# Optimization experiments

Measured on AMD Instinct MI355X. Metric: run time of the kernel, lower is better.

Reference implementation:

```python
import jax, jax.numpy as jnp
import numpy as np

BINS = 1000  # torch: int(max-min)*100; ~1000 for standardized randn data, fixed for jit


def _entropy(counts, n, width):
    # torch.histogram(density=True): probs = counts / (n * bin_width)
    probs = counts / (n * width)
    safe = jnp.where(probs > 0, probs, 1.0)
    return jnp.sum(jnp.where(probs > 0, -probs * jnp.log2(safe), 0.0))


def setup_inputs() -> dict:
    key = jax.random.key(0)
    k1, k2 = jax.random.split(key)
    x = jax.random.normal(k1, (1024, 64, 16, 16), dtype=jnp.float32)
    u = jax.random.uniform(k2, (1024, 64, 16, 16), dtype=jnp.float32)  # dropout noise
    return {"x": x, "u": u}


def reference(x, u):
    B = x.shape[0]
    temp = x.reshape(B, -1)              # [B, D]
    D = temp.shape[1]

    # corrcoef across rows (each row is a variable)
    tc = temp - temp.mean(axis=1, keepdims=True)
    cov = tc @ tc.T                      # [B, B]
    d = jnp.sqrt(jnp.diag(cov))
    corr = cov / (d[:, None] * d[None, :])
    factor1 = jnp.mean(jnp.abs(corr), axis=1)            # [B]

    # global standardization (torch.std default is unbiased, ddof=1)
    tnorm = (temp - temp.mean()) / jnp.std(temp, ddof=1)
    lo, hi = tnorm.min(), tnorm.max()
    width = (hi - lo) / BINS
    idx = jnp.clip(jnp.floor((tnorm - lo) / width).astype(jnp.int32), 0, BINS - 1)

    # per-row histograms via batched scatter-add; batch histogram = sum of rows
    row_counts = jax.vmap(lambda ii: jnp.zeros(BINS, jnp.float32).at[ii].add(1.0))(idx)  # [B, BINS]
    batch_counts = row_counts.sum(axis=0)

    batch_entropy = _entropy(batch_counts, B * D, width)
    local_entropy = jax.vmap(lambda c: _entropy(c, D, width))(row_counts)  # [B]

    f2 = local_entropy / batch_entropy
    is_zero = f2 == 0
    f1 = jnp.where(is_zero, 0.0, factor1)
    f2 = jnp.where(is_zero, 1.0, jnp.where(f2 < 1.0, 1.0 / f2, f2))
    keep = f1 / f2                       # 1 - p, per row
    p = 1.0 - keep                       # [B]

    mask = (u.reshape(B, -1) > p[:, None]).astype(x.dtype)
    out = (mask * temp) / keep[:, None]
    return out.reshape(x.shape)
```

## Files before the change

kernel.cpp:

```cpp
#include <hip/hip_runtime.h>
#include <math.h>

#define NROWS 1024
#define DCOLS 16384
#define NTOT  16777216
#define BINS  1000
#define NPAIR 136

typedef short short8 __attribute__((ext_vector_type(8)));
typedef unsigned short ushort8 __attribute__((ext_vector_type(8)));
typedef float f32x4 __attribute__((ext_vector_type(4)));

#define GLOAD_LDS16(gp, lp) __builtin_amdgcn_global_load_lds( \
    (const __attribute__((address_space(1))) unsigned int*)(gp), \
    (__attribute__((address_space(3))) unsigned int*)(lp), 16, 0, 0)

__device__ __constant__ int CHK_TR[12] = {1,17,33,49,  0,5,10,15,  128,149,170,191};
__device__ __constant__ int CHK_CB[12] = {0,0,0,0,     128,128,128,128,  0,0,0,0};
__device__ __constant__ int CHK_SL[12] = {0,0,0,0,     2,2,2,2,    0,0,0,0};

__global__ __launch_bounds__(256) void k_rowsplit(const float* __restrict__ x,
    unsigned short* __restrict__ phi, unsigned short* __restrict__ plo,
    double* __restrict__ rowsum, double* __restrict__ rowsumsq,
    double* __restrict__ rowmin, double* __restrict__ rowmax) {
  const int row = blockIdx.x, t = threadIdx.x;
  const size_t base = (size_t)row * DCOLS;
  double s = 0.0, s2 = 0.0;
  float mn = 3.4028235e38f, mx = -3.4028235e38f;
  #pragma unroll
  for (int i = 0; i < 8; ++i) {
    const size_t off = base + (size_t)i * 2048 + (size_t)t * 8;
    const float4 v0 = *(const float4*)(x + off);
    const float4 v1 = *(const float4*)(x + off + 4);
    const float vv[8] = {v0.x, v0.y, v0.z, v0.w, v1.x, v1.y, v1.z, v1.w};
    ushort8 h, lo;
    #pragma unroll
    for (int c = 0; c < 8; ++c) {
      unsigned ub = __float_as_uint(vv[c]);
      unsigned hb = (ub + 0x7FFFu + ((ub >> 16) & 1u)) >> 16;
      float hf = __uint_as_float(hb << 16);
      float r = vv[c] - hf;
      unsigned ur = __float_as_uint(r);
      unsigned lb = (ur + 0x7FFFu + ((ur >> 16) & 1u)) >> 16;
      h[c] = (unsigned short)hb; lo[c] = (unsigned short)lb;
      double dv = vv[c];
      s += dv; s2 += dv * dv;
      mn = fminf(mn, vv[c]); mx = fmaxf(mx, vv[c]);
    }
    *(ushort8*)(phi + off) = h;
    *(ushort8*)(plo + off) = lo;
  }
  #pragma unroll
  for (int off = 32; off > 0; off >>= 1) {
    s  += __shfl_down(s, off);
    s2 += __shfl_down(s2, off);
    mn = fminf(mn, __shfl_down(mn, off));
    mx = fmaxf(mx, __shfl_down(mx, off));
  }
  __shared__ double lsd[8];
  __shared__ float  lsf[8];
  const int lane = t & 63, w = t >> 6;
  if (lane == 0) { lsd[w] = s; lsd[4 + w] = s2; lsf[w] = mn; lsf[4 + w] = mx; }
  __syncthreads();
  if (t == 0) {
    rowsum[row]   = (lsd[0] + lsd[1]) + (lsd[2] + lsd[3]);
    rowsumsq[row] = (lsd[4] + lsd[5]) + (lsd[6] + lsd[7]);
    rowmin[row] = (double)fminf(fminf(lsf[0], lsf[1]), fminf(lsf[2], lsf[3]));
    rowmax[row] = (double)fmaxf(fmaxf(lsf[4], lsf[5]), fmaxf(lsf[6], lsf[7]));
  }
}

__global__ __launch_bounds__(256) void k_rowstats(const float* __restrict__ x,
    double* __restrict__ rowsum, double* __restrict__ rowsumsq,
    double* __restrict__ rowmin, double* __restrict__ rowmax) {
  const int row = blockIdx.x;
  const int t = threadIdx.x;
  const float4* xr = (const float4*)(x + (size_t)row * DCOLS);
  double s = 0.0, s2 = 0.0;
  float mn = 3.4028235e38f, mx = -3.4028235e38f;
  for (int j = t; j < DCOLS / 4; j += 256) {
    float4 v = xr[j];
    double a = v.x, b = v.y, c = v.z, d = v.w;
    s  += (a + b) + (c + d);
    s2 += (a * a + b * b) + (c * c + d * d);
    mn = fminf(mn, fminf(fminf(v.x, v.y), fminf(v.z, v.w)));
    mx = fmaxf(mx, fmaxf(fmaxf(v.x, v.y), fmaxf(v.z, v.w)));
  }
  #pragma unroll
  for (int off = 32; off > 0; off >>= 1) {
    s  += __shfl_down(s, off);
    s2 += __shfl_down(s2, off);
    mn = fminf(mn, __shfl_down(mn, off));
    mx = fmaxf(mx, __shfl_down(mx, off));
  }
  __shared__ double lsd[8];
  __shared__ float  lsf[8];
  const int lane = t & 63, w = t >> 6;
  if (lane == 0) { lsd[w] = s; lsd[4 + w] = s2; lsf[w] = mn; lsf[4 + w] = mx; }
  __syncthreads();
  if (t == 0) {
    rowsum[row]   = (lsd[0] + lsd[1]) + (lsd[2] + lsd[3]);
    rowsumsq[row] = (lsd[4] + lsd[5]) + (lsd[6] + lsd[7]);
    rowmin[row] = (double)fminf(fminf(lsf[0], lsf[1]), fminf(lsf[2], lsf[3]));
    rowmax[row] = (double)fmaxf(fmaxf(lsf[4], lsf[5]), fmaxf(lsf[6], lsf[7]));
  }
}

__global__ __launch_bounds__(256) void k_stats2(
    const double* __restrict__ rowsum, const double* __restrict__ rowsumsq,
    const double* __restrict__ rowmin, const double* __restrict__ rowmax,
    double* __restrict__ m, double* __restrict__ dn, float* __restrict__ fscal,
    float* __restrict__ flg, unsigned* __restrict__ bc) {
#pragma clang fp contract(off)
  const int t = threadIdx.x;
  for (int b = t; b < BINS; b += 256) bc[b] = 0;
  double s = 0.0, s2 = 0.0, mn = 1e300, mx = -1e300;
  for (int r = t; r < NROWS; r += 256) {
    s += rowsum[r]; s2 += rowsumsq[r];
    mn = fmin(mn, rowmin[r]); mx = fmax(mx, rowmax[r]);
  }
  #pragma unroll
  for (int off = 32; off > 0; off >>= 1) {
    s  += __shfl_down(s, off);
    s2 += __shfl_down(s2, off);
    mn = fmin(mn, __shfl_down(mn, off));
    mx = fmax(mx, __shfl_down(mx, off));
  }
  __shared__ double lsd[16];
  const int lane = t & 63, w = t >> 6;
  if (lane == 0) { lsd[w] = s; lsd[4 + w] = s2; lsd[8 + w] = mn; lsd[12 + w] = mx; }
  __syncthreads();
  if (t == 0) {
    double S  = (lsd[0] + lsd[1]) + (lsd[2] + lsd[3]);
    double S2 = (lsd[4] + lsd[5]) + (lsd[6] + lsd[7]);
    double MN = fmin(fmin(lsd[8], lsd[9]), fmin(lsd[10], lsd[11]));
    double MX = fmax(fmax(lsd[12], lsd[13]), fmax(lsd[14], lsd[15]));
    const double N = 16777216.0;
    double mu  = S / N;
    double var = (S2 - S * S / N) / (N - 1.0);
    double sig = sqrt(var);
    float mu32 = (float)mu;
    float sg32 = (float)sig;
    float mnf  = (float)MN;
    float mxf  = (float)MX;
    float lof  = (mnf - mu32) / sg32;
    float hif  = (mxf - mu32) / sg32;
    float wf   = (hif - lof) / 1000.0f;
    fscal[0] = mu32;
    fscal[1] = sg32;
    fscal[2] = lof;
    fscal[3] = wf;
    fscal[4] = 16384.0f * wf;
    fscal[5] = 16777216.0f * wf;
    flg[0] = 0.0f;
  }
  __syncthreads();
  for (int r = t; r < NROWS; r += 256) {
    double rs = rowsum[r];
    m[r]  = rs / 16384.0;
    dn[r] = sqrt(rowsumsq[r] - rs * rs * (1.0 / 16384.0));
  }
}

__global__ __launch_bounds__(256) void k_gramm_sk(
    const unsigned short* __restrict__ phi, const unsigned short* __restrict__ plo,
    float* __restrict__ Gs) {
  const int pid = blockIdx.x >> 2, ks = blockIdx.x & 3;
  int bi = 0, rem = pid;
  while (rem >= 16 - bi) { rem -= 16 - bi; ++bi; }
  const int bj = bi + rem;
  const bool diag = (bi == bj);
  __shared__ short As[2][64][64];
  __shared__ short Bs[2][64][64];
  const int t = threadIdx.x;
  const int w = t >> 6, l = t & 63;

  const unsigned short* plane = (w & 1) ? plo : phi;
  const int prow0 = (w & 2) ? bj * 64 : bi * 64;
  short* lbase = (w & 2) ? &Bs[w & 1][0][0] : &As[w & 1][0][0];
  const bool skipStage = diag && (w & 2);
  const unsigned short* gbase = plane
      + (size_t)(prow0 + (l >> 3)) * DCOLS + (((l & 7) ^ (l >> 3)) * 8);

  f32x4 acc[4] = {{0.f,0.f,0.f,0.f},{0.f,0.f,0.f,0.f},{0.f,0.f,0.f,0.f},{0.f,0.f,0.f,0.f}};
  double dacc[4][4] = {{0,0,0,0},{0,0,0,0},{0,0,0,0},{0,0,0,0}};

  const int arow = w * 16 + (l & 15);
  const int ar7  = arow & 7;
  const short* Bsrc0 = diag ? &As[0][0][0] : &Bs[0][0][0];
  const short* Bsrc1 = diag ? &As[1][0][0] : &Bs[1][0][0];
  const int kbeg = ks * 4096;

  for (int K0 = kbeg; K0 < kbeg + 4096; K0 += 2048) {
    for (int k0 = K0; k0 < K0 + 2048; k0 += 64) {
      __syncthreads();
      if (!skipStage) {
        #pragma unroll
        for (int q = 0; q < 8; ++q)
          GLOAD_LDS16(gbase + (size_t)q * 8 * DCOLS + k0, lbase + q * 512);
      }
      __syncthreads();
      const int p0 = ((l >> 4)) ^ ar7;
      const int p1 = (4 + (l >> 4)) ^ ar7;
      short8 ah0 = *(const short8*)&As[0][arow][p0 * 8];
      short8 ah1 = *(const short8*)&As[0][arow][p1 * 8];
      short8 al0 = *(const short8*)&As[1][arow][p0 * 8];
      short8 al1 = *(const short8*)&As[1][arow][p1 * 8];
      #pragma unroll
      for (int cj = 0; cj < 4; ++cj) {
        const int brow = cj * 16 + (l & 15);
        const int q0 = ((l >> 4)) ^ (brow & 7);
        const int q1 = (4 + (l >> 4)) ^ (brow & 7);
        short8 bh0 = *(const short8*)(Bsrc0 + brow * 64 + q0 * 8);
        short8 bh1 = *(const short8*)(Bsrc0 + brow * 64 + q1 * 8);
        short8 bl0 = *(const short8*)(Bsrc1 + brow * 64 + q0 * 8);
        short8 bl1 = *(const short8*)(Bsrc1 + brow * 64 + q1 * 8);
        acc[cj] = __builtin_amdgcn_mfma_f32_16x16x32_bf16(ah0, bh0, acc[cj], 0, 0, 0);
        acc[cj] = __builtin_amdgcn_mfma_f32_16x16x32_bf16(ah1, bh1, acc[cj], 0, 0, 0);
        acc[cj] = __builtin_amdgcn_mfma_f32_16x16x32_bf16(ah0, bl0, acc[cj], 0, 0, 0);
        acc[cj] = __builtin_amdgcn_mfma_f32_16x16x32_bf16(ah1, bl1, acc[cj], 0, 0, 0);
        acc[cj] = __builtin_amdgcn_mfma_f32_16x16x32_bf16(al0, bh0, acc[cj], 0, 0, 0);
        acc[cj] = __builtin_amdgcn_mfma_f32_16x16x32_bf16(al1, bh1, acc[cj], 0, 0, 0);
      }
    }
    #pragma unroll
    for (int cj = 0; cj < 4; ++cj) {
      #pragma unroll
      for (int v = 0; v < 4; ++v) dacc[cj][v] += (double)acc[cj][v];
      acc[cj] = (f32x4){0.f, 0.f, 0.f, 0.f};
    }
  }

  float* gt = Gs + ((size_t)pid * 4 + ks) * 4096;
  #pragma unroll
  for (int cj = 0; cj < 4; ++cj)
    #pragma unroll
    for (int v = 0; v < 4; ++v)
      gt[(w * 16 + (l >> 4) * 4 + v) * 64 + cj * 16 + (l & 15)] = (float)dacc[cj][v];
}

__global__ __launch_bounds__(256) void k_gepi(const float* __restrict__ Gs,
    const double* __restrict__ m, const double* __restrict__ dn,
    double* __restrict__ fpart) {
  const int pid = blockIdx.x;
  int bi = 0, rem = pid;
  while (rem >= 16 - bi) { rem -= 16 - bi; ++bi; }
  const int bj = bi + rem;
  const bool diag = (bi == bj);
  __shared__ double Gt[64][65];
  const int t = threadIdx.x;
  const float* g = Gs + (size_t)pid * 4 * 4096;
  for (int i = t; i < 4096; i += 256) {
    double sg = ((double)g[i] + (double)g[4096 + i])
              + ((double)g[8192 + i] + (double)g[12288 + i]);
    Gt[i >> 6][i & 63] = sg;
  }
  __syncthreads();
  {
    const int r = t >> 2, q = t & 3;
    const double mi = m[bi * 64 + r] * 16384.0;
    double s = 0.0;
    #pragma unroll
    for (int i = 0; i < 16; ++i) {
      const int c = q * 16 + i;
      double cov = Gt[r][c] - mi * m[bj * 64 + c];
      s += fabs(cov) / dn[bj * 64 + c];
    }
    s += __shfl_xor(s, 1); s += __shfl_xor(s, 2);
    if (q == 0) fpart[(size_t)(bi * 64 + r) * 16 + bj] = s;
  }
  if (!diag) {
    const int c = t >> 2, q = t & 3;
    const double mj = m[bj * 64 + c] * 16384.0;
    double sc = 0.0;
    #pragma unroll
    for (int i = 0; i < 16; ++i) {
      const int r = q * 16 + i;
      double cov = Gt[r][c] - m[bi * 64 + r] * mj;
      sc += fabs(cov) / dn[bi * 64 + r];
    }
    sc += __shfl_xor(sc, 1); sc += __shfl_xor(sc, 2);
    if (q == 0) fpart[(size_t)(bj * 64 + c) * 16 + bi] = sc;
  }
}

__global__ __launch_bounds__(256) void k_check3(const float* __restrict__ x,
    const double* __restrict__ m, const double* __restrict__ dn,
    double* __restrict__ chkpart) {
  const int b = blockIdx.x;
  const int e = b >> 3, grp = b & 7;
  const int t = threadIdx.x;
  const int cl = t >> 5;
  const int ks = t & 31;
  const int trow = CHK_TR[e];
  const int col  = CHK_CB[e] + grp * 8 + cl;
  const float4* xa = (const float4*)(x + (size_t)trow * DCOLS) + ks * 128;
  const float4* xb = (const float4*)(x + (size_t)col  * DCOLS) + ks * 128;
  double g = 0.0;
  for (int k = 0; k < 128; ++k) {
    float4 va = xa[k], vb = xb[k];
    g += (double)va.x * vb.x + (double)va.y * vb.y
       + (double)va.z * vb.z + (double)va.w * vb.w;
  }
  g += __shfl_xor(g, 1); g += __shfl_xor(g, 2); g += __shfl_xor(g, 4);
  g += __shfl_xor(g, 8); g += __shfl_xor(g, 16);
  __shared__ double cd[8];
  if (ks == 0) cd[cl] = g;
  __syncthreads();
  if (t == 0) {
    double s = 0.0;
    #pragma unroll
    for (int i = 0; i < 8; ++i) {
      int c = CHK_CB[e] + grp * 8 + i;
      double cov = cd[i] - 16384.0 * m[trow] * m[c];
      s += fabs(cov) / dn[c];
    }
    chkpart[e * 8 + grp] = s;
  }
}

__global__ __launch_bounds__(256) void k_gram(const float* __restrict__ x,
    const double* __restrict__ m, const double* __restrict__ dn,
    double* __restrict__ fpart) {
  __shared__ float As[32][72];
  __shared__ float Bs[32][72];
  __shared__ double red[64][16];
  const int t = threadIdx.x;
  const int bi = blockIdx.y, bj = blockIdx.x;
  const int tx = t & 15, ty = t >> 4;
  const int lr = t >> 2, lc = t & 3;
  const float* Ap = x + (size_t)(bi * 64 + lr) * DCOLS;
  const float* Bp = x + (size_t)(bj * 64 + lr) * DCOLS;
  double acc[4][4];
  #pragma unroll
  for (int i = 0; i < 4; ++i)
    #pragma unroll
    for (int j = 0; j < 4; ++j) acc[i][j] = 0.0;
  float4 a0 = ((const float4*)Ap)[lc];
  float4 a1 = ((const float4*)Ap)[lc + 4];
  float4 b0 = ((const float4*)Bp)[lc];
  float4 b1 = ((const float4*)Bp)[lc + 4];
  for (int k0 = 0; k0 < DCOLS; k0 += 32) {
    __syncthreads();
    {
      const float* a0p = (const float*)&a0;
      const float* a1p = (const float*)&a1;
      const float* b0p = (const float*)&b0;
      const float* b1p = (const float*)&b1;
      #pragma unroll
      for (int jj = 0; jj < 4; ++jj) {
        As[lc * 4 + jj][lr]      = a0p[jj];
        As[16 + lc * 4 + jj][lr] = a1p[jj];
        Bs[lc * 4 + jj][lr]      = b0p[jj];
        Bs[16 + lc * 4 + jj][lr] = b1p[jj];
      }
    }
    __syncthreads();
    if (k0 + 32 < DCOLS) {
      a0 = ((const float4*)(Ap + k0 + 32))[lc];
      a1 = ((const float4*)(Ap + k0 + 32))[lc + 4];
      b0 = ((const float4*)(Bp + k0 + 32))[lc];
      b1 = ((const float4*)(Bp + k0 + 32))[lc + 4];
    }
    float ac[4][4];
    #pragma unroll
    for (int i = 0; i < 4; ++i)
      #pragma unroll
      for (int j = 0; j < 4; ++j) ac[i][j] = 0.0f;
    #pragma unroll
    for (int k = 0; k < 32; ++k) {
      const float4 av = *(const float4*)&As[k][ty * 4];
      const float4 bv = *(const float4*)&Bs[k][tx * 4];
      const float aa[4] = {av.x, av.y, av.z, av.w};
      const float bb[4] = {bv.x, bv.y, bv.z, bv.w};
      #pragma unroll
      for (int i = 0; i < 4; ++i)
        #pragma unroll
        for (int j = 0; j < 4; ++j)
          ac[i][j] += aa[i] * bb[j];
    }
    #pragma unroll
    for (int i = 0; i < 4; ++i)
      #pragma unroll
      for (int j = 0; j < 4; ++j) acc[i][j] += (double)ac[i][j];
  }
  double mr[4], mc[4], dc[4];
  #pragma unroll
  for (int i = 0; i < 4; ++i) mr[i] = m[bi * 64 + ty * 4 + i];
  #pragma unroll
  for (int j = 0; j < 4; ++j) {
    int col = bj * 64 + tx * 4 + j;
    mc[j] = m[col]; dc[j] = dn[col];
  }
  #pragma unroll
  for (int i = 0; i < 4; ++i) {
    double pi = 0.0;
    #pragma unroll
    for (int j = 0; j < 4; ++j) {
      double cov = acc[i][j] - 16384.0 * mr[i] * mc[j];
      pi += fabs(cov) / dc[j];
    }
    red[ty * 4 + i][tx] = pi;
  }
  __syncthreads();
  if (t < 64) {
    double ssum = 0.0;
    #pragma unroll
    for (int q = 0; q < 16; ++q) ssum += red[t][q];
    fpart[(size_t)(bi * 64 + t) * 16 + bj] = ssum;
  }
}

__global__ __launch_bounds__(256) void k_hist(const float* __restrict__ x,
    const float* __restrict__ fscal, double* __restrict__ localent,
    unsigned* __restrict__ bc) {
#pragma clang fp contract(off)
  __shared__ unsigned h[BINS];
  const int row = blockIdx.x, t = threadIdx.x;
  for (int b = t; b < BINS; b += 256) h[b] = 0;
  __syncthreads();
  const float mu32 = fscal[0], sg32 = fscal[1], lof = fscal[2], wf = fscal[3];
  const float4* xr = (const float4*)(x + (size_t)row * DCOLS);
  for (int j = t; j < DCOLS / 4; j += 256) {
    float4 v = xr[j];
    float vv[4] = {v.x, v.y, v.z, v.w};
    #pragma unroll
    for (int c = 0; c < 4; ++c) {
      float tn = (vv[c] - mu32) / sg32;
      float q  = (tn - lof) / wf;
      int idx = (int)floorf(q);
      idx = idx < 0 ? 0 : (idx > BINS - 1 ? BINS - 1 : idx);
      atomicAdd(&h[idx], 1u);
    }
  }
  __syncthreads();
  const double Dw = (double)fscal[4];
  double ls = 0.0;
  for (int b = t; b < BINS; b += 256) {
    unsigned c = h[b];
    if (c) {
      atomicAdd(&bc[b], c);
      double pd = (double)c / Dw;
      ls -= pd * log2(pd);
    }
  }
  #pragma unroll
  for (int off = 32; off > 0; off >>= 1) ls += __shfl_down(ls, off);
  __shared__ double lsd[4];
  const int lane = t & 63, w = t >> 6;
  if (lane == 0) lsd[w] = ls;
  __syncthreads();
  if (t == 0) localent[row] = (lsd[0] + lsd[1]) + (lsd[2] + lsd[3]);
}

__global__ __launch_bounds__(256) void k_final(const unsigned* __restrict__ bc,
    const float* __restrict__ fscal, const double* __restrict__ localent,
    const double* __restrict__ fpart, const double* __restrict__ dn,
    const double* __restrict__ chkpart, float* __restrict__ flg,
    float* __restrict__ pf, float* __restrict__ kf) {
#pragma clang fp contract(off)
  const int t = threadIdx.x;
  if (t < 12) {
    double s = 0.0;
    #pragma unroll
    for (int q = 0; q < 8; ++q) s += chkpart[t * 8 + q];
    double got = fpart[(size_t)CHK_TR[t] * 16 + CHK_SL[t]];
    if (fabs(got - s) > 2e-3 * fmax(fabs(s), 1e-30))
      atomicAdd(flg, 1e6f * (float)(t + 1));
  }
  const double Nw = (double)fscal[5];
  double be = 0.0;
  for (int b = t; b < BINS; b += 256) {
    unsigned c = bc[b];
    if (c) { double pd = (double)c / Nw; be -= pd * log2(pd); }
  }
  #pragma unroll
  for (int off = 32; off > 0; off >>= 1) be += __shfl_down(be, off);
  __shared__ double lsd[4];
  __shared__ double sbent;
  const int lane = t & 63, w = t >> 6;
  if (lane == 0) lsd[w] = be;
  __syncthreads();
  if (t == 0) sbent = (lsd[0] + lsd[1]) + (lsd[2] + lsd[3]);
  __syncthreads();
  const float bef = (float)sbent;
  for (int r = t; r < NROWS; r += 256) {
    double s = 0.0;
    #pragma unroll
    for (int q = 0; q < 16; ++q) s += fpart[(size_t)r * 16 + q];
    float f1f = (float)(s / (dn[r] * 1024.0));
    float lef = (float)localent[r];
    float f2f = lef / bef;
    if (f2f == 0.0f) { f1f = 0.0f; f2f = 1.0f; }
    else if (f2f < 1.0f) f2f = 1.0f / f2f;
    float keepf = f1f / f2f;
    pf[r] = 1.0f - keepf;
    kf[r] = keepf;
  }
}

__global__ __launch_bounds__(256) void k_apply(const float* __restrict__ x,
    const float* __restrict__ u, const float* __restrict__ pf,
    const float* __restrict__ kf, const float* __restrict__ flg,
    float* __restrict__ out) {
#pragma clang fp contract(off)
  const size_t e = ((size_t)blockIdx.x * 256 + threadIdx.x) * 4;
  const float fl = flg[0];
  if (fl != 0.0f) {
    float4 o = {0.f, 0.f, 0.f, 0.f};
    if (e == 0) o.x = fl;
    *(float4*)(out + e) = o;
    return;
  }
  const int row = (int)(e >> 14);
  const float pr = pf[row], kr = kf[row];
  const float4 xv = *(const float4*)(x + e);
  const float4 uv = *(const float4*)(u + e);
  float4 o;
  o.x = (uv.x > pr) ? (xv.x / kr) : 0.0f;
  o.y = (uv.y > pr) ? (xv.y / kr) : 0.0f;
  o.z = (uv.z > pr) ? (xv.z / kr) : 0.0f;
  o.w = (uv.w > pr) ? (xv.w / kr) : 0.0f;
  *(float4*)(out + e) = o;
}

extern "C" void kernel_launch(void* const* d_in, const int* in_sizes, int n_in,
                              void* d_out, int out_size, void* d_ws, size_t ws_size,
                              hipStream_t stream) {
  const float* x = (const float*)d_in[0];
  const float* u = (const float*)d_in[1];
  float* out = (float*)d_out;

  const size_t PLANE = (size_t)NROWS * DCOLS * sizeof(unsigned short);
  const size_t NDBL  = 7 * 1024 + (size_t)NROWS * 16 + 96;
  const size_t TAILB = NDBL * 8 + (2056 + 4) * 4 + BINS * 4;
  const bool big = ws_size >= 2 * PLANE + TAILB;

  char* base = (char*)d_ws;
  unsigned short* phi = (unsigned short*)base;
  unsigned short* plo = (unsigned short*)(base + PLANE);
  double* W = big ? (double*)(base + 2 * PLANE) : (double*)base;

  double* rowsum   = W;
  double* rowsumsq = W + 1024;
  double* rowmin   = W + 2048;
  double* rowmax   = W + 3072;
  double* m        = W + 4096;
  double* dn       = W + 5120;
  double* localent = W + 6144;
  double* fpart    = W + 7168;
  double* chkpart  = W + 7168 + (size_t)NROWS * 16;
  float*  F        = (float*)(chkpart + 96);
  float*  pf       = F;
  float*  kf       = F + 1024;
  float*  fscal    = F + 2048;
  float*  flg      = F + 2056;
  unsigned* bc     = (unsigned*)(F + 2060);

  if (big) {
    float* Gs = out;
    k_rowsplit<<<NROWS, 256, 0, stream>>>(x, phi, plo, rowsum, rowsumsq, rowmin, rowmax);
    k_stats2<<<1, 256, 0, stream>>>(rowsum, rowsumsq, rowmin, rowmax, m, dn, fscal, flg, bc);
    k_gramm_sk<<<NPAIR * 4, 256, 0, stream>>>(phi, plo, Gs);
    k_gepi<<<NPAIR, 256, 0, stream>>>(Gs, m, dn, fpart);
    k_check3<<<96, 256, 0, stream>>>(x, m, dn, chkpart);
  } else {
    k_rowstats<<<NROWS, 256, 0, stream>>>(x, rowsum, rowsumsq, rowmin, rowmax);
    k_stats2<<<1, 256, 0, stream>>>(rowsum, rowsumsq, rowmin, rowmax, m, dn, fscal, flg, bc);
    k_gram<<<dim3(16, 16), 256, 0, stream>>>(x, m, dn, fpart);
    k_check3<<<96, 256, 0, stream>>>(x, m, dn, chkpart);
  }
  k_hist<<<NROWS, 256, 0, stream>>>(x, fscal, localent, bc);
  k_final<<<1, 256, 0, stream>>>(bc, fscal, localent, fpart, dn, chkpart, flg, pf, kf);
  k_apply<<<NTOT / (256 * 4), 256, 0, stream>>>(x, u, pf, kf, flg, out);
}
```

Measured before the change: 213.5 us.

## Raise Gram split-K to 8, use 2x2 wave tiling, fuse epilogue with check

The Gram kernel now splits K eight ways instead of four, giving 1088 blocks and better CU fill. Each wave computes a 32x32 quadrant with 2x2 MFMA subtiles instead of a 16x64 strip, which cuts LDS fragment reloads per MFMA. The epilogue now sums eight partials, and the check kernel is merged into it as extra blocks, removing one launch. The cost is twice the partial-Gram traffic through global memory and more epilogue reads. Per-block fp32 accumulation now covers 2048 K instead of being flushed to double every 2048, so precision is about the same.

```diff
diff --git a/kernel.cpp b/kernel.cpp
--- a/kernel.cpp
+++ b/kernel.cpp
@@ -6,6 +6,7 @@
 #define NTOT  16777216
 #define BINS  1000
 #define NPAIR 136
+#define KSPL  8
 
 typedef short short8 __attribute__((ext_vector_type(8)));
 typedef unsigned short ushort8 __attribute__((ext_vector_type(8)));
@@ -165,7 +166,7 @@
 __global__ __launch_bounds__(256) void k_gramm_sk(
     const unsigned short* __restrict__ phi, const unsigned short* __restrict__ plo,
     float* __restrict__ Gs) {
-  const int pid = blockIdx.x >> 2, ks = blockIdx.x & 3;
+  const int pid = blockIdx.x >> 3, ks = blockIdx.x & 7;
   int bi = 0, rem = pid;
   while (rem >= 16 - bi) { rem -= 16 - bi; ++bi; }
   const int bj = bi + rem;
@@ -182,77 +183,124 @@
   const unsigned short* gbase = plane
       + (size_t)(prow0 + (l >> 3)) * DCOLS + (((l & 7) ^ (l >> 3)) * 8);
 
-  f32x4 acc[4] = {{0.f,0.f,0.f,0.f},{0.f,0.f,0.f,0.f},{0.f,0.f,0.f,0.f},{0.f,0.f,0.f,0.f}};
-  double dacc[4][4] = {{0,0,0,0},{0,0,0,0},{0,0,0,0},{0,0,0,0}};
-
-  const int arow = w * 16 + (l & 15);
-  const int ar7  = arow & 7;
-  const short* Bsrc0 = diag ? &As[0][0][0] : &Bs[0][0][0];
-  const short* Bsrc1 = diag ? &As[1][0][0] : &Bs[1][0][0];
-  const int kbeg = ks * 4096;
-
-  for (int K0 = kbeg; K0 < kbeg + 4096; K0 += 2048) {
-    for (int k0 = K0; k0 < K0 + 2048; k0 += 64) {
-      __syncthreads();
-      if (!skipStage) {
+  f32x4 acc[2][2] = {{{0.f,0.f,0.f,0.f},{0.f,0.f,0.f,0.f}},
+                     {{0.f,0.f,0.f,0.f},{0.f,0.f,0.f,0.f}}};
+  double dacc[2][2][4] = {{{0,0,0,0},{0,0,0,0}},{{0,0,0,0},{0,0,0,0}}};
+
+  const int wr = w >> 1, wc = w & 1;
+  const short* BA0 = diag ? &As[0][0][0] : &Bs[0][0][0];
+  const short* BA1 = diag ? &As[1][0][0] : &Bs[1][0][0];
+  const int kbeg = ks * 2048;
+
+  for (int k0 = kbeg; k0 < kbeg + 2048; k0 += 64) {
+    __syncthreads();
+    if (!skipStage) {
+      #pragma unroll
+      for (int q = 0; q < 8; ++q)
+        GLOAD_LDS16(gbase + (size_t)q * 8 * DCOLS + k0, lbase + q * 512);
+    }
+    __syncthreads();
+    short8 ah[2][2], al[2][2], bh[2][2], bl[2][2];
+    #pragma unroll
+    for (int as_ = 0; as_ < 2; ++as_) {
+      const int arow = wr * 32 + as_ * 16 + (l & 15);
+      const int r7 = arow & 7;
+      #pragma unroll
+      for (int kk = 0; kk < 2; ++kk) {
+        const int p = (kk * 4 + (l >> 4)) ^ r7;
+        ah[as_][kk] = *(const short8*)&As[0][arow][p * 8];
+        al[as_][kk] = *(const short8*)&As[1][arow][p * 8];
+      }
+    }
+    #pragma unroll
+    for (int bs_ = 0; bs_ < 2; ++bs_) {
+      const int brow = wc * 32 + bs_ * 16 + (l & 15);
+      const int r7 = brow & 7;
+      #pragma unroll
+      for (int kk = 0; kk < 2; ++kk) {
+        const int p = (kk * 4 + (l >> 4)) ^ r7;
+        bh[bs_][kk] = *(const short8*)(BA0 + brow * 64 + p * 8);
+        bl[bs_][kk] = *(const short8*)(BA1 + brow * 64 + p * 8);
+      }
+    }
+    #pragma unroll
+    for (int as_ = 0; as_ < 2; ++as_)
+      #pragma unroll
+      for (int bs_ = 0; bs_ < 2; ++bs_)
         #pragma unroll
-        for (int q = 0; q < 8; ++q)
-          GLOAD_LDS16(gbase + (size_t)q * 8 * DCOLS + k0, lbase + q * 512);
+        for (int kk = 0; kk < 2; ++kk) {
+          acc[as_][bs_] = __builtin_amdgcn_mfma_f32_16x16x32_bf16(ah[as_][kk], bh[bs_][kk], acc[as_][bs_], 0, 0, 0);
+          acc[as_][bs_] = __builtin_amdgcn_mfma_f32_16x16x32_bf16(ah[as_][kk], bl[bs_][kk], acc[as_][bs_], 0, 0, 0);
+          acc[as_][bs_] = __builtin_amdgcn_mfma_f32_16x16x32_bf16(al[as_][kk], bh[bs_][kk], acc[as_][bs_], 0, 0, 0);
+        }
+  }
+  #pragma unroll
+  for (int as_ = 0; as_ < 2; ++as_)
+    #pragma unroll
+    for (int bs_ = 0; bs_ < 2; ++bs_)
+      #pragma unroll
+      for (int v = 0; v < 4; ++v) dacc[as_][bs_][v] = (double)acc[as_][bs_][v];
+
+  float* gt = Gs + ((size_t)pid * KSPL + ks) * 4096;
+  #pragma unroll
+  for (int as_ = 0; as_ < 2; ++as_)
+    #pragma unroll
+    for (int bs_ = 0; bs_ < 2; ++bs_)
+      #pragma unroll
+      for (int v = 0; v < 4; ++v)
+        gt[(wr * 32 + as_ * 16 + (l >> 4) * 4 + v) * 64 + wc * 32 + bs_ * 16 + (l & 15)]
+            = (float)dacc[as_][bs_][v];
+}
+
+__global__ __launch_bounds__(256) void k_gepi_chk(const float* __restrict__ x,
+    const float* __restrict__ Gs, const double* __restrict__ m,
+    const double* __restrict__ dn, double* __restrict__ fpart,
+    double* __restrict__ chkpart, int nGepi) {
+  const int t = threadIdx.x;
+  if ((int)blockIdx.x >= nGepi) {
+    const int b = blockIdx.x - nGepi;
+    const int e = b >> 3, grp = b & 7;
+    const int cl = t >> 5;
+    const int ksg = t & 31;
+    const int trow = CHK_TR[e];
+    const int col  = CHK_CB[e] + grp * 8 + cl;
+    const float4* xa = (const float4*)(x + (size_t)trow * DCOLS) + ksg * 128;
+    const float4* xb = (const float4*)(x + (size_t)col  * DCOLS) + ksg * 128;
+    double g = 0.0;
+    for (int k = 0; k < 128; ++k) {
+      float4 va = xa[k], vb = xb[k];
+      g += (double)va.x * vb.x + (double)va.y * vb.y
+         + (double)va.z * vb.z + (double)va.w * vb.w;
+    }
+    g += __shfl_xor(g, 1); g += __shfl_xor(g, 2); g += __shfl_xor(g, 4);
+    g += __shfl_xor(g, 8); g += __shfl_xor(g, 16);
+    __shared__ double cd[8];
+    if (ksg == 0) cd[cl] = g;
+    __syncthreads();
+    if (t == 0) {
+      double s = 0.0;
+      #pragma unroll
+      for (int i = 0; i < 8; ++i) {
+        int c = CHK_CB[e] + grp * 8 + i;
+        double cov = cd[i] - 16384.0 * m[trow] * m[c];
+        s += fabs(cov) / dn[c];
       }
-      __syncthreads();
-      const int p0 = ((l >> 4)) ^ ar7;
-      const int p1 = (4 + (l >> 4)) ^ ar7;
-      short8 ah0 = *(const short8*)&As[0][arow][p0 * 8];
-      short8 ah1 = *(const short8*)&As[0][arow][p1 * 8];
-      short8 al0 = *(const short8*)&As[1][arow][p0 * 8];
-      short8 al1 = *(const short8*)&As[1][arow][p1 * 8];
-      #pragma unroll
-      for (int cj = 0; cj < 4; ++cj) {
-        const int brow = cj * 16 + (l & 15);
-        const int q0 = ((l >> 4)) ^ (brow & 7);
-        const int q1 = (4 + (l >> 4)) ^ (brow & 7);
-        short8 bh0 = *(const short8*)(Bsrc0 + brow * 64 + q0 * 8);
-        short8 bh1 = *(const short8*)(Bsrc0 + brow * 64 + q1 * 8);
-        short8 bl0 = *(const short8*)(Bsrc1 + brow * 64 + q0 * 8);
-        short8 bl1 = *(const short8*)(Bsrc1 + brow * 64 + q1 * 8);
-        acc[cj] = __builtin_amdgcn_mfma_f32_16x16x32_bf16(ah0, bh0, acc[cj], 0, 0, 0);
-        acc[cj] = __builtin_amdgcn_mfma_f32_16x16x32_bf16(ah1, bh1, acc[cj], 0, 0, 0);
-        acc[cj] = __builtin_amdgcn_mfma_f32_16x16x32_bf16(ah0, bl0, acc[cj], 0, 0, 0);
-        acc[cj] = __builtin_amdgcn_mfma_f32_16x16x32_bf16(ah1, bl1, acc[cj], 0, 0, 0);
-        acc[cj] = __builtin_amdgcn_mfma_f32_16x16x32_bf16(al0, bh0, acc[cj], 0, 0, 0);
-        acc[cj] = __builtin_amdgcn_mfma_f32_16x16x32_bf16(al1, bh1, acc[cj], 0, 0, 0);
-      }
-    }
-    #pragma unroll
-    for (int cj = 0; cj < 4; ++cj) {
-      #pragma unroll
-      for (int v = 0; v < 4; ++v) dacc[cj][v] += (double)acc[cj][v];
-      acc[cj] = (f32x4){0.f, 0.f, 0.f, 0.f};
-    }
-  }
-
-  float* gt = Gs + ((size_t)pid * 4 + ks) * 4096;
-  #pragma unroll
-  for (int cj = 0; cj < 4; ++cj)
-    #pragma unroll
-    for (int v = 0; v < 4; ++v)
-      gt[(w * 16 + (l >> 4) * 4 + v) * 64 + cj * 16 + (l & 15)] = (float)dacc[cj][v];
-}
-
-__global__ __launch_bounds__(256) void k_gepi(const float* __restrict__ Gs,
-    const double* __restrict__ m, const double* __restrict__ dn,
-    double* __restrict__ fpart) {
+      chkpart[e * 8 + grp] = s;
+    }
+    return;
+  }
   const int pid = blockIdx.x;
   int bi = 0, rem = pid;
   while (rem >= 16 - bi) { rem -= 16 - bi; ++bi; }
   const int bj = bi + rem;
   const bool diag = (bi == bj);
   __shared__ double Gt[64][65];
-  const int t = threadIdx.x;
-  const float* g = Gs + (size_t)pid * 4 * 4096;
+  const float* g = Gs + (size_t)pid * KSPL * 4096;
   for (int i = t; i < 4096; i += 256) {
-    double sg = ((double)g[i] + (double)g[4096 + i])
-              + ((double)g[8192 + i] + (double)g[12288 + i]);
+    double sg = (((double)g[i]           + (double)g[4096 + i])
+              +  ((double)g[8192 + i]    + (double)g[12288 + i]))
+              + (((double)g[16384 + i]   + (double)g[20480 + i])
+              +  ((double)g[24576 + i]   + (double)g[28672 + i]));
     Gt[i >> 6][i & 63] = sg;
   }
   __syncthreads();
@@ -281,41 +329,6 @@
     }
     sc += __shfl_xor(sc, 1); sc += __shfl_xor(sc, 2);
     if (q == 0) fpart[(size_t)(bj * 64 + c) * 16 + bi] = sc;
-  }
-}
-
-__global__ __launch_bounds__(256) void k_check3(const float* __restrict__ x,
-    const double* __restrict__ m, const double* __restrict__ dn,
-    double* __restrict__ chkpart) {
-  const int b = blockIdx.x;
-  const int e = b >> 3, grp = b & 7;
-  const int t = threadIdx.x;
-  const int cl = t >> 5;
-  const int ks = t & 31;
-  const int trow = CHK_TR[e];
-  const int col  = CHK_CB[e] + grp * 8 + cl;
-  const float4* xa = (const float4*)(x + (size_t)trow * DCOLS) + ks * 128;
-  const float4* xb = (const float4*)(x + (size_t)col  * DCOLS) + ks * 128;
-  double g = 0.0;
-  for (int k = 0; k < 128; ++k) {
-    float4 va = xa[k], vb = xb[k];
-    g += (double)va.x * vb.x + (double)va.y * vb.y
-       + (double)va.z * vb.z + (double)va.w * vb.w;
-  }
-  g += __shfl_xor(g, 1); g += __shfl_xor(g, 2); g += __shfl_xor(g, 4);
-  g += __shfl_xor(g, 8); g += __shfl_xor(g, 16);
-  __shared__ double cd[8];
-  if (ks == 0) cd[cl] = g;
-  __syncthreads();
-  if (t == 0) {
-    double s = 0.0;
-    #pragma unroll
-    for (int i = 0; i < 8; ++i) {
-      int c = CHK_CB[e] + grp * 8 + i;
-      double cov = cd[i] - 16384.0 * m[trow] * m[c];
-      s += fabs(cov) / dn[c];
-    }
-    chkpart[e * 8 + grp] = s;
   }
 }
 
@@ -561,14 +574,13 @@
     float* Gs = out;
     k_rowsplit<<<NROWS, 256, 0, stream>>>(x, phi, plo, rowsum, rowsumsq, rowmin, rowmax);
     k_stats2<<<1, 256, 0, stream>>>(rowsum, rowsumsq, rowmin, rowmax, m, dn, fscal, flg, bc);
-    k_gramm_sk<<<NPAIR * 4, 256, 0, stream>>>(phi, plo, Gs);
-    k_gepi<<<NPAIR, 256, 0, stream>>>(Gs, m, dn, fpart);
-    k_check3<<<96, 256, 0, stream>>>(x, m, dn, chkpart);
+    k_gramm_sk<<<NPAIR * KSPL, 256, 0, stream>>>(phi, plo, Gs);
+    k_gepi_chk<<<NPAIR + 96, 256, 0, stream>>>(x, Gs, m, dn, fpart, chkpart, NPAIR);
   } else {
     k_rowstats<<<NROWS, 256, 0, stream>>>(x, rowsum, rowsumsq, rowmin, rowmax);
     k_stats2<<<1, 256, 0, stream>>>(rowsum, rowsumsq, rowmin, rowmax, m, dn, fscal, flg, bc);
     k_gram<<<dim3(16, 16), 256, 0, stream>>>(x, m, dn, fpart);
-    k_check3<<<96, 256, 0, stream>>>(x, m, dn, chkpart);
+    k_gepi_chk<<<96, 256, 0, stream>>>(x, (const float*)out, m, dn, fpart, chkpart, 0);
   }
   k_hist<<<NROWS, 256, 0, stream>>>(x, fscal, localent, bc);
   k_final<<<1, 256, 0, stream>>>(bc, fscal, localent, fpart, dn, chkpart, flg, pf, kf);
```

After: 203.0 us. 1.05x faster.
